# Optimization experiments

Measured on AMD Instinct MI355X. Metric: run time of the kernel, lower is better.

Reference implementation:

```python
import jax, jax.numpy as jnp
import numpy as np

LN_EPS = 1e-5
DEG_EPS = 1e-6
H = 256
N_VAR = 100000
NUM_CON = 50000
E = 300000


def setup_inputs() -> dict:
    key = jax.random.key(0)
    ks = jax.random.split(key, 8)
    s = 1.0 / np.sqrt(H)
    s2 = 1.0 / np.sqrt(H + 1)
    return {
        "x_var": jax.random.normal(ks[0], (N_VAR, H), dtype=jnp.float32),
        "src": jax.random.randint(ks[1], (E,), 0, N_VAR, dtype=jnp.int32),
        "dst": jax.random.randint(ks[2], (E,), 0, NUM_CON, dtype=jnp.int32),
        "clue_values": jax.random.normal(ks[3], (NUM_CON,), dtype=jnp.float32),
        "num_con": NUM_CON,
        "msg_W": jax.random.uniform(ks[4], (H, H), jnp.float32, -s, s),
        "msg_b": jax.random.uniform(ks[5], (H,), jnp.float32, -s, s),
        "update_W": jax.random.uniform(ks[6], (H, H + 1), jnp.float32, -s2, s2),
        "update_b": jax.random.uniform(ks[7], (H,), jnp.float32, -s2, s2),
        "ln_w": jnp.ones((H,), jnp.float32),
        "ln_b": jnp.zeros((H,), jnp.float32),
    }


def reference(x_var, src, dst, clue_values, num_con, msg_W, msg_b, update_W, update_b, ln_w, ln_b):
    # gather + linear message transform: (E, H)
    msgs = x_var[src] @ msg_W.T + msg_b
    # degree-normalized scatter-add into constraints: (num_con, H)
    agg = jax.ops.segment_sum(msgs, dst, num_segments=num_con)
    deg = jax.ops.segment_sum(jnp.ones((dst.shape[0],), msgs.dtype), dst, num_segments=num_con)
    agg = agg / (deg[:, None] + DEG_EPS)
    # concat clue scalar, update MLP, ReLU
    h = jnp.concatenate([agg, clue_values[:, None]], axis=1)
    out = jax.nn.relu(h @ update_W.T + update_b)
    # LayerNorm over last dim
    mu = out.mean(axis=-1, keepdims=True)
    var = out.var(axis=-1, keepdims=True)
    return (out - mu) * jax.lax.rsqrt(var + LN_EPS) * ln_w + ln_b
```

## Files before the change

### kernel.cpp

```cpp
#include <hip/hip_runtime.h>

#define HD 256
#define LN_EPS 1e-5f
#define DEG_EPS 1e-6f
#define CAP 64
#define CY 264

typedef __attribute__((ext_vector_type(8))) short short8;
typedef __attribute__((ext_vector_type(4))) short s16x4;
typedef __attribute__((ext_vector_type(4))) float f32x4;
typedef __attribute__((ext_vector_type(4))) int i32x4;

__device__ inline unsigned short f2bf(float f) {
    union { float f; unsigned int u; } v; v.f = f;
    unsigned int r = v.u + 0x7FFFu + ((v.u >> 16) & 1u);
    return (unsigned short)(r >> 16);
}
__device__ inline float bf2f(unsigned short h) {
    union { unsigned int u; float f; } v; v.u = ((unsigned int)h) << 16;
    return v.f;
}
__device__ inline short8 cvt8(float4 u0, float4 u1) {
    short8 o;
    o[0] = (short)f2bf(u0.x); o[1] = (short)f2bf(u0.y);
    o[2] = (short)f2bf(u0.z); o[3] = (short)f2bf(u0.w);
    o[4] = (short)f2bf(u1.x); o[5] = (short)f2bf(u1.y);
    o[6] = (short)f2bf(u1.z); o[7] = (short)f2bf(u1.w);
    return o;
}

__global__ __launch_bounds__(256) void prep0_kernel(
    int* __restrict__ counts, int num_con,
    const float* __restrict__ msg_W, const float* __restrict__ msg_b,
    const float* __restrict__ upd_W,
    unsigned short* __restrict__ w12b, float* __restrict__ bv,
    float* __restrict__ ucol, int zb) {
    int b = blockIdx.x, tid = threadIdx.x;
    if (b < zb) {
        int i = (b * 256 + tid) * 4;
        if (i + 4 <= num_con) *(i32x4*)(counts + i) = (i32x4){0, 0, 0, 0};
        else for (; i < num_con; ++i) counts[i] = 0;
    } else {
        int j = b - zb, k = tid;
        float a0 = 0.f, a1 = 0.f, a2 = 0.f, a3 = 0.f, accb = 0.f;
#pragma unroll 2
        for (int m = 0; m < 256; m += 4) {
            float w0 = upd_W[j * 257 + m + 0];
            float w1 = upd_W[j * 257 + m + 1];
            float w2 = upd_W[j * 257 + m + 2];
            float w3 = upd_W[j * 257 + m + 3];
            a0 = fmaf(w0, msg_W[(m + 0) * 256 + k], a0);
            a1 = fmaf(w1, msg_W[(m + 1) * 256 + k], a1);
            a2 = fmaf(w2, msg_W[(m + 2) * 256 + k], a2);
            a3 = fmaf(w3, msg_W[(m + 3) * 256 + k], a3);
            accb = fmaf(w0, msg_b[m + 0], accb);
            accb = fmaf(w1, msg_b[m + 1], accb);
            accb = fmaf(w2, msg_b[m + 2], accb);
            accb = fmaf(w3, msg_b[m + 3], accb);
        }
        w12b[j * 256 + k] = f2bf((a0 + a1) + (a2 + a3));
        if (k == 0) { bv[j] = accb; ucol[j] = upd_W[j * 257 + 256]; }
    }
}

__global__ __launch_bounds__(256) void fill_kernel(
    const int* __restrict__ src, const int* __restrict__ dst,
    int* __restrict__ counts, int* __restrict__ eidx, int E) {
    int e = blockIdx.x * 256 + threadIdx.x;
    if (e >= E) return;
    int d = dst[e];
    int p = atomicAdd(&counts[d], 1);
    if (p < CAP) eidx[d * CAP + p] = src[e];
}

__global__ __launch_bounds__(256) void ygemm_kernel(
    const float* __restrict__ x, const unsigned short* __restrict__ w12b,
    unsigned short* __restrict__ y, int n_var, int ntiles) {

    __shared__ unsigned short sA[16 * 256];
    __shared__ unsigned short sY[2][16 * CY];
    const int tid = threadIdx.x, w = tid >> 6, lane = tid & 63;
    const int lr = lane & 15, lg = lane >> 4;

    short8 bfr[4][8];
#pragma unroll
    for (int jt = 0; jt < 4; ++jt)
#pragma unroll
        for (int ks = 0; ks < 8; ++ks)
            bfr[jt][ks] = *(const short8*)(w12b + (w * 64 + jt * 16 + lr) * HD + lg * 8 + ks * 32);

    const int srow = tid >> 4, scol = (tid & 15) * 16;

    int buf = 0;
#pragma unroll 1
    for (int rt = blockIdx.x; rt < ntiles; rt += gridDim.x) {
        int r0 = rt * 16;
        {
            int arc = min(r0 + srow, n_var - 1);
            const float* gp = x + (long)arc * HD + scol;
            float4 u0 = *(const float4*)(gp);
            float4 u1 = *(const float4*)(gp + 4);
            float4 u2 = *(const float4*)(gp + 8);
            float4 u3 = *(const float4*)(gp + 12);
            int b0 = (srow * 512 + scol * 2) ^ ((srow & 7) << 4);
            int b1 = (srow * 512 + scol * 2 + 16) ^ ((srow & 7) << 4);
            *(short8*)((char*)sA + b0) = cvt8(u0, u1);
            *(short8*)((char*)sA + b1) = cvt8(u2, u3);
        }
        __syncthreads();

        short8 af[8];
#pragma unroll
        for (int ks = 0; ks < 8; ++ks) {
            int byte = (lr * 512 + (ks * 32 + lg * 8) * 2) ^ ((lr & 7) << 4);
            af[ks] = *(const short8*)((char*)sA + byte);
        }

        f32x4 acc[4] = {{0.f,0.f,0.f,0.f},{0.f,0.f,0.f,0.f},{0.f,0.f,0.f,0.f},{0.f,0.f,0.f,0.f}};
#pragma unroll
        for (int ks = 0; ks < 8; ++ks)
#pragma unroll
            for (int jt = 0; jt < 4; ++jt)
                acc[jt] = __builtin_amdgcn_mfma_f32_16x16x32_bf16(af[ks], bfr[jt][ks], acc[jt], 0, 0, 0);

#pragma unroll
        for (int jt = 0; jt < 4; ++jt)
#pragma unroll
            for (int q = 0; q < 4; ++q) {
                unsigned short mb = f2bf(acc[jt][q]);
                int nb = __shfl_xor((int)(unsigned int)mb, 1, 64);
                if (!(lr & 1)) {
                    unsigned int pk = (unsigned int)mb | (((unsigned int)nb & 0xFFFFu) << 16);
                    *(unsigned int*)((char*)&sY[buf][0] +
                        ((lg * 4 + q) * CY + w * 64 + jt * 16 + lr) * 2) = pk;
                }
            }
        __syncthreads();
        {
            int grow = r0 + srow;
            if (grow < n_var) {
                const unsigned short* sp = &sY[buf][srow * CY + scol];
                short8 v0 = *(const short8*)(sp);
                short8 v1 = *(const short8*)(sp + 8);
                unsigned short* gp = y + (long)grow * HD + scol;
                *(short8*)gp = v0;
                *(short8*)(gp + 8) = v1;
            }
        }
        buf ^= 1;
    }
}

__global__ __launch_bounds__(256) void gatherln_kernel(
    const unsigned short* __restrict__ y, const int* __restrict__ counts,
    const int* __restrict__ eidx, const float* __restrict__ clue,
    const float* __restrict__ bv, const float* __restrict__ ucol,
    const float* __restrict__ upd_b,
    const float* __restrict__ ln_w, const float* __restrict__ ln_b,
    float* __restrict__ out, int num_con) {
    int row  = blockIdx.x * 4 + (threadIdx.x >> 6);
    int lane = threadIdx.x & 63;
    if (row >= num_con) return;
    int cnt = counts[row];
    int cgo = min(cnt, CAP);
    int sid = (lane < cgo) ? eidx[row * CAP + lane] : 0;
    float a0 = 0.f, a1 = 0.f, a2 = 0.f, a3 = 0.f;
#pragma unroll 1
    for (int i = 0; i < cgo; i += 8) {
        int s[8];
#pragma unroll
        for (int u = 0; u < 8; ++u) s[u] = __shfl(sid, i + u, 64);
        s16x4 v[8];
#pragma unroll
        for (int u = 0; u < 8; ++u)
            v[u] = *(const s16x4*)(y + (long)s[u] * HD + lane * 4);
#pragma unroll
        for (int u = 0; u < 8; ++u) {
            float wg = (i + u < cgo) ? 1.f : 0.f;
            a0 = fmaf(bf2f((unsigned short)v[u][0]), wg, a0);
            a1 = fmaf(bf2f((unsigned short)v[u][1]), wg, a1);
            a2 = fmaf(bf2f((unsigned short)v[u][2]), wg, a2);
            a3 = fmaf(bf2f((unsigned short)v[u][3]), wg, a3);
        }
    }
    float sc = 1.0f / ((float)cnt + DEG_EPS);
    float tc = (float)cnt * sc;
    float cl = clue[row];
    f32x4 bvv = *(const f32x4*)(bv + lane * 4);
    f32x4 uc4 = *(const f32x4*)(ucol + lane * 4);
    f32x4 b24 = *(const f32x4*)(upd_b + lane * 4);
    float z0 = fmaxf(a0 * sc + tc * bvv[0] + cl * uc4[0] + b24[0], 0.0f);
    float z1 = fmaxf(a1 * sc + tc * bvv[1] + cl * uc4[1] + b24[1], 0.0f);
    float z2 = fmaxf(a2 * sc + tc * bvv[2] + cl * uc4[2] + b24[2], 0.0f);
    float z3 = fmaxf(a3 * sc + tc * bvv[3] + cl * uc4[3] + b24[3], 0.0f);
    float s  = z0 + z1 + z2 + z3;
    float s2 = z0 * z0 + z1 * z1 + z2 * z2 + z3 * z3;
#pragma unroll
    for (int m = 1; m < 64; m <<= 1) {
        s  += __shfl_xor(s,  m, 64);
        s2 += __shfl_xor(s2, m, 64);
    }
    float mu = s * (1.0f / HD);
    float var = s2 * (1.0f / HD) - mu * mu;
    float rs = rsqrtf(var + LN_EPS);
    f32x4 lw = *(const f32x4*)(ln_w + lane * 4);
    f32x4 lb = *(const f32x4*)(ln_b + lane * 4);
    float4 o;
    o.x = (z0 - mu) * rs * lw[0] + lb[0];
    o.y = (z1 - mu) * rs * lw[1] + lb[1];
    o.z = (z2 - mu) * rs * lw[2] + lb[2];
    o.w = (z3 - mu) * rs * lw[3] + lb[3];
    *(float4*)(out + (long)row * HD + lane * 4) = o;
}

extern "C" void kernel_launch(void* const* d_in, const int* in_sizes, int n_in,
                              void* d_out, int out_size, void* d_ws, size_t ws_size,
                              hipStream_t stream) {
    const float* x_var = (const float*)d_in[0];
    const int*   src   = (const int*)d_in[1];
    const int*   dst   = (const int*)d_in[2];
    const float* clue  = (const float*)d_in[3];
    const float* msg_W = (const float*)d_in[5];
    const float* msg_b = (const float*)d_in[6];
    const float* upd_W = (const float*)d_in[7];
    const float* upd_b = (const float*)d_in[8];
    const float* ln_w  = (const float*)d_in[9];
    const float* ln_b  = (const float*)d_in[10];

    int E = in_sizes[1];
    long n_x = in_sizes[0];
    int n_var = (int)(n_x / HD);
    int num_con = out_size / HD;
    int ntiles_v = (n_var + 15) / 16;

    char* ws = (char*)d_ws;
    int* counts = (int*)ws;
    int* eidx   = (int*)(ws + (((size_t)num_con * 4 + 255) & ~(size_t)255));
    char* after = (char*)(eidx + (size_t)num_con * CAP);
    size_t yoff = ((size_t)(after - ws) + 255) & ~(size_t)255;
    unsigned short* yv = (unsigned short*)(ws + yoff);
    size_t woff = (yoff + (size_t)n_var * HD * 2 + 255) & ~(size_t)255;
    unsigned short* w12b = (unsigned short*)(ws + woff);
    float* bvp  = (float*)(w12b + 256 * 256);
    float* ucol = bvp + 256;

    int zb = (num_con + 1023) / 1024;
    prep0_kernel<<<zb + 256, 256, 0, stream>>>(
        counts, num_con, msg_W, msg_b, upd_W, w12b, bvp, ucol, zb);

    fill_kernel<<<(E + 255) / 256, 256, 0, stream>>>(src, dst, counts, eidx, E);

    ygemm_kernel<<<2048, 256, 0, stream>>>(x_var, w12b, yv, n_var, ntiles_v);

    gatherln_kernel<<<(num_con + 3) / 4, 256, 0, stream>>>(
        yv, counts, eidx, clue, bvp, ucol, upd_b, ln_w, ln_b,
        (float*)d_out, num_con);
}
```

Before: 121.5 us.

## Store GEMM output in permuted column order to drop LDS staging

The y-GEMM kernel no longer stages its bf16 results through a shared-memory transpose buffer with shuffles and an extra barrier. Each lane now writes its four MFMA outputs directly as one 8-byte store, so y columns are stored in a permuted order, and the shared A tile is double-buffered. The gather/LayerNorm kernel is changed to match: it maps each lane's four accumulated values back to their logical columns when reading bias, update and LN parameters and when writing the output. This trades the extra sync and LDS traffic for scalar strided loads of the parameter vectors and 4-byte scattered output stores instead of float4 stores.

```diff
diff --git a/kernel.cpp b/kernel.cpp
--- a/kernel.cpp
+++ b/kernel.cpp
@@ -4,7 +4,6 @@
 #define LN_EPS 1e-5f
 #define DEG_EPS 1e-6f
 #define CAP 64
-#define CY 264
 
 typedef __attribute__((ext_vector_type(8))) short short8;
 typedef __attribute__((ext_vector_type(4))) short s16x4;
@@ -77,8 +76,7 @@
     const float* __restrict__ x, const unsigned short* __restrict__ w12b,
     unsigned short* __restrict__ y, int n_var, int ntiles) {
 
-    __shared__ unsigned short sA[16 * 256];
-    __shared__ unsigned short sY[2][16 * CY];
+    __shared__ unsigned short sA[2][16 * 256];
     const int tid = threadIdx.x, w = tid >> 6, lane = tid & 63;
     const int lr = lane & 15, lg = lane >> 4;
 
@@ -104,8 +102,8 @@
             float4 u3 = *(const float4*)(gp + 12);
             int b0 = (srow * 512 + scol * 2) ^ ((srow & 7) << 4);
             int b1 = (srow * 512 + scol * 2 + 16) ^ ((srow & 7) << 4);
-            *(short8*)((char*)sA + b0) = cvt8(u0, u1);
-            *(short8*)((char*)sA + b1) = cvt8(u2, u3);
+            *(short8*)((char*)&sA[buf][0] + b0) = cvt8(u0, u1);
+            *(short8*)((char*)&sA[buf][0] + b1) = cvt8(u2, u3);
         }
         __syncthreads();
 
@@ -113,7 +111,7 @@
 #pragma unroll
         for (int ks = 0; ks < 8; ++ks) {
             int byte = (lr * 512 + (ks * 32 + lg * 8) * 2) ^ ((lr & 7) << 4);
-            af[ks] = *(const short8*)((char*)sA + byte);
+            af[ks] = *(const short8*)((char*)&sA[buf][0] + byte);
         }
 
         f32x4 acc[4] = {{0.f,0.f,0.f,0.f},{0.f,0.f,0.f,0.f},{0.f,0.f,0.f,0.f},{0.f,0.f,0.f,0.f}};
@@ -124,27 +122,13 @@
                 acc[jt] = __builtin_amdgcn_mfma_f32_16x16x32_bf16(af[ks], bfr[jt][ks], acc[jt], 0, 0, 0);
 
 #pragma unroll
-        for (int jt = 0; jt < 4; ++jt)
-#pragma unroll
-            for (int q = 0; q < 4; ++q) {
-                unsigned short mb = f2bf(acc[jt][q]);
-                int nb = __shfl_xor((int)(unsigned int)mb, 1, 64);
-                if (!(lr & 1)) {
-                    unsigned int pk = (unsigned int)mb | (((unsigned int)nb & 0xFFFFu) << 16);
-                    *(unsigned int*)((char*)&sY[buf][0] +
-                        ((lg * 4 + q) * CY + w * 64 + jt * 16 + lr) * 2) = pk;
-                }
-            }
-        __syncthreads();
-        {
-            int grow = r0 + srow;
+        for (int q = 0; q < 4; ++q) {
+            int grow = r0 + lg * 4 + q;
             if (grow < n_var) {
-                const unsigned short* sp = &sY[buf][srow * CY + scol];
-                short8 v0 = *(const short8*)(sp);
-                short8 v1 = *(const short8*)(sp + 8);
-                unsigned short* gp = y + (long)grow * HD + scol;
-                *(short8*)gp = v0;
-                *(short8*)(gp + 8) = v1;
+                s16x4 o;
+#pragma unroll
+                for (int jt = 0; jt < 4; ++jt) o[jt] = (short)f2bf(acc[jt][q]);
+                *(s16x4*)(y + (long)grow * HD + w * 64 + lr * 4) = o;
             }
         }
         buf ^= 1;
@@ -183,18 +167,19 @@
             a3 = fmaf(bf2f((unsigned short)v[u][3]), wg, a3);
         }
     }
+    int c0 = ((lane >> 4) << 6) + (lane & 15);
     float sc = 1.0f / ((float)cnt + DEG_EPS);
     float tc = (float)cnt * sc;
     float cl = clue[row];
-    f32x4 bvv = *(const f32x4*)(bv + lane * 4);
-    f32x4 uc4 = *(const f32x4*)(ucol + lane * 4);
-    f32x4 b24 = *(const f32x4*)(upd_b + lane * 4);
-    float z0 = fmaxf(a0 * sc + tc * bvv[0] + cl * uc4[0] + b24[0], 0.0f);
-    float z1 = fmaxf(a1 * sc + tc * bvv[1] + cl * uc4[1] + b24[1], 0.0f);
-    float z2 = fmaxf(a2 * sc + tc * bvv[2] + cl * uc4[2] + b24[2], 0.0f);
-    float z3 = fmaxf(a3 * sc + tc * bvv[3] + cl * uc4[3] + b24[3], 0.0f);
-    float s  = z0 + z1 + z2 + z3;
-    float s2 = z0 * z0 + z1 * z1 + z2 * z2 + z3 * z3;
+    float z[4] = {a0, a1, a2, a3};
+    float s = 0.f, s2 = 0.f;
+#pragma unroll
+    for (int jt = 0; jt < 4; ++jt) {
+        int c = c0 + jt * 16;
+        float zz = fmaxf(z[jt] * sc + tc * bv[c] + cl * ucol[c] + upd_b[c], 0.0f);
+        z[jt] = zz;
+        s += zz; s2 += zz * zz;
+    }
 #pragma unroll
     for (int m = 1; m < 64; m <<= 1) {
         s  += __shfl_xor(s,  m, 64);
@@ -203,14 +188,12 @@
     float mu = s * (1.0f / HD);
     float var = s2 * (1.0f / HD) - mu * mu;
     float rs = rsqrtf(var + LN_EPS);
-    f32x4 lw = *(const f32x4*)(ln_w + lane * 4);
-    f32x4 lb = *(const f32x4*)(ln_b + lane * 4);
-    float4 o;
-    o.x = (z0 - mu) * rs * lw[0] + lb[0];
-    o.y = (z1 - mu) * rs * lw[1] + lb[1];
-    o.z = (z2 - mu) * rs * lw[2] + lb[2];
-    o.w = (z3 - mu) * rs * lw[3] + lb[3];
-    *(float4*)(out + (long)row * HD + lane * 4) = o;
+    float* gp = out + (long)row * HD;
+#pragma unroll
+    for (int jt = 0; jt < 4; ++jt) {
+        int c = c0 + jt * 16;
+        gp[c] = (z[jt] - mu) * rs * ln_w[c] + ln_b[c];
+    }
 }
 
 extern "C" void kernel_launch(void* const* d_in, const int* in_sizes, int n_in,
```

Result: faster. 111.4 us (-8.2%).
